# Performance work log

Measured on AMD Instinct MI355X. Metric: run time of the kernel, lower is better.

## Reference

```python
import jax, jax.numpy as jnp
import numpy as np

B, S, H = 16, 128, 768
L, K = 2, 4
NORM_ITEM = 0.5


def _xavier(key, shape):
    fan_in, fan_out = shape[-1], shape[-2]
    std = float(np.sqrt(2.0 / (fan_in + fan_out)))
    return jax.random.normal(key, shape, dtype=jnp.float32) * std


def setup_inputs() -> dict:
    key = jax.random.key(0)
    ks = jax.random.split(key, 13)
    sentences = jax.random.normal(ks[0], (B, S, H), dtype=jnp.float32)
    adj_matrix = jax.random.uniform(ks[1], (B, K, S, S), dtype=jnp.float32)
    return {
        "sentences": sentences,
        "adj_matrix": adj_matrix,
        # stacked per-(layer, dep_kind) parameters
        "W_in": _xavier(ks[2], (L, K, H, H)),
        "b_in": _xavier(ks[3], (L, K, H, 1)),
        "W_out": _xavier(ks[4], (L, K, H, H)),
        "b_out": _xavier(ks[5], (L, K, H, 1)),
        "Wg_in": _xavier(ks[6], (L, K, H, H)),
        "bg_in": _xavier(ks[7], (L, K, H, 1)),
        "Wg_out": _xavier(ks[8], (L, K, H, H)),
        "bg_out": _xavier(ks[9], (L, K, H, 1)),
        "W_loop": _xavier(ks[10], (L, H, H)),
    }


def reference(sentences, adj_matrix, W_in, b_in, W_out, b_out,
              Wg_in, bg_in, Wg_out, bg_out, W_loop):
    # sentences: [B,S,H], adj_matrix: [B,K,S,S]
    adj_in = adj_matrix                       # message along edges
    adj_out = jnp.swapaxes(adj_matrix, 2, 3)  # reversed edges
    h = jnp.swapaxes(sentences, 1, 2)         # [B,H,S]

    def conv(Wg, bg, W, b, adj, h):
        # Wg,W: [K,H,H]; bg,b: [K,H,1]; adj: [B,K,S,S]; h: [B,H,S]
        gate = jax.nn.sigmoid(jnp.einsum('khd,bds->bkhs', Wg, h) + bg[None])
        rel = NORM_ITEM * gate * (jnp.einsum('khd,bds->bkhs', W, h) + b[None])
        # bmm with adjacency, then sum over dep kinds
        return jnp.einsum('bkhs,bkst->bht', rel, adj)

    n_layers = W_in.shape[0]
    for l in range(n_layers):
        s = jnp.einsum('hd,bds->bhs', W_loop[l], h)  # self loop
        s = s + conv(Wg_in[l], bg_in[l], W_in[l], b_in[l], adj_in, h)
        s = s + conv(Wg_out[l], bg_out[l], W_out[l], b_out[l], adj_out, h)
        h = jax.nn.relu(s)
    return jnp.swapaxes(h, 1, 2)  # [B,S,H]
```

## Files before the change

### kernel.cpp

```cpp
#include <hip/hip_runtime.h>
#include <stdint.h>

#define B_ 16
#define S_ 128
#define H_ 768
#define K_ 4
#define L_ 2
#define T_ (B_*S_)

typedef __attribute__((ext_vector_type(4))) float f32x4;
typedef __attribute__((ext_vector_type(8))) short s16x8;
typedef __bf16 bf16x8 __attribute__((ext_vector_type(8)));
typedef unsigned short u16;

__device__ inline u16 f2bf(float f) {
    union { float f; uint32_t u; } v; v.f = f;
    uint32_t u = v.u;
    return (u16)((u + 0x7fffu + ((u >> 16) & 1u)) >> 16);
}

__device__ inline ushort4 f2bf4(float4 v) {
    ushort4 r; r.x = f2bf(v.x); r.y = f2bf(v.y); r.z = f2bf(v.z); r.w = f2bf(v.w);
    return r;
}

template <typename T>
__device__ inline auto mfma_impl(T a, T b, f32x4 c, int)
    -> decltype(__builtin_amdgcn_mfma_f32_16x16x32_bf16(a, b, c, 0, 0, 0)) {
    return __builtin_amdgcn_mfma_f32_16x16x32_bf16(a, b, c, 0, 0, 0);
}
template <typename T>
__device__ inline f32x4 mfma_impl(T a, T b, f32x4 c, long) {
    return __builtin_amdgcn_mfma_f32_16x16x32_bf16(
        __builtin_bit_cast(bf16x8, a), __builtin_bit_cast(bf16x8, b), c, 0, 0, 0);
}
__device__ inline f32x4 mfma16(s16x8 a, s16x8 b, f32x4 c) {
    return mfma_impl(a, b, c, 0);
}

__device__ inline void gload_lds16(const void* g, void* l) {
    __builtin_amdgcn_global_load_lds(
        (__attribute__((address_space(1))) void*)(g),
        (__attribute__((address_space(3))) void*)(l), 16, 0, 0);
}

__device__ inline void stage_tile(const char* gbase, int rowStrideBytes, u16* lds, int tid) {
    const int lane = tid & 63;
    const int w = tid >> 6;
    const int lr = lane >> 3;
    const int cb = (lane & 7) << 4;
    #pragma unroll
    for (int j = 0; j < 4; ++j) {
        const int seg = j * 4 + w;
        const int row = seg * 8 + lr;
        const int sb = cb ^ ((row & 7) << 4);
        gload_lds16(gbase + (size_t)row * rowStrideBytes + sb,
                    lds + seg * 512);
    }
}

__device__ inline void stage64(const char* gbase, int rowStrideBytes, char* lds, int tid) {
    const int lane = tid & 63;
    const int w = tid >> 6;
    const int lr = lane >> 3;
    const int cb = (lane & 7) << 4;
    #pragma unroll
    for (int j = 0; j < 2; ++j) {
        const int seg = j * 4 + w;
        const int row = seg * 8 + lr;
        const int sb = cb ^ ((row & 7) << 4);
        gload_lds16(gbase + (size_t)row * rowStrideBytes + sb,
                    lds + seg * 1024);
    }
}

__device__ inline void stage128(const char* gRow0, int rowStrideBytes, char* ldsBase, int tid) {
    const int lane = tid & 63;
    const int w = tid >> 6;
    const int lr = lane >> 3;
    #pragma unroll
    for (int j = 0; j < 2; ++j) {
        const int seg = w * 2 + j;
        const int row = seg * 8 + lr;
        const int sb = ((lane & 7) << 4) ^ ((row & 7) << 4);
        gload_lds16(gRow0 + (size_t)row * rowStrideBytes + sb,
                    ldsBase + seg * 1024);
    }
}

__device__ inline s16x8 read_frag(const u16* lds, int row, int colByte) {
    const int bir = colByte ^ ((row & 7) << 4);
    return *(const s16x8*)((const char*)lds + row * 128 + bir);
}

__global__ void prep_weights(const float* __restrict__ Wg_in, const float* __restrict__ Wg_out,
                             const float* __restrict__ W_in,  const float* __restrict__ W_out,
                             const float* __restrict__ W_loop, const float* __restrict__ sent,
                             u16* __restrict__ Wg_all, u16* __restrict__ W_all,
                             u16* __restrict__ Wl, u16* __restrict__ X0) {
    const int i4 = blockIdx.x * blockDim.x + threadIdx.x;
    const int NW4 = L_ * K_ * H_ * H_ / 4;
    const int KHH4 = K_ * H_ * H_ / 4;
    if (i4 < NW4) {
        const int l = i4 / KHH4;
        const int rem = i4 - l * KHH4;
        const int d0 = (l * 2) * KHH4 + rem;
        const int d1 = d0 + KHH4;
        ((ushort4*)Wg_all)[d0] = f2bf4(((const float4*)Wg_in)[i4]);
        ((ushort4*)Wg_all)[d1] = f2bf4(((const float4*)Wg_out)[i4]);
        ((ushort4*)W_all)[d0]  = f2bf4(((const float4*)W_in)[i4]);
        ((ushort4*)W_all)[d1]  = f2bf4(((const float4*)W_out)[i4]);
    }
    if (i4 < L_ * H_ * H_ / 4)  ((ushort4*)Wl)[i4] = f2bf4(((const float4*)W_loop)[i4]);
    if (i4 < T_ * H_ / 4)       ((ushort4*)X0)[i4] = f2bf4(((const float4*)sent)[i4]);
}

__global__ void prep_adj(const float* __restrict__ adj, u16* __restrict__ adjA) {
    const int idx = blockIdx.x * blockDim.x + threadIdx.x;
    const int s = idx & 127;
    const int t = (idx >> 7) & 127;
    const int b = (idx >> 14) & 15;
    const int p = idx >> 18;
    const int dir = p >> 2, k = p & 3;
    const float v = dir ? adj[(((size_t)b * K_ + k) * S_ + t) * S_ + s]
                        : adj[(((size_t)b * K_ + k) * S_ + s) * S_ + t];
    adjA[idx] = f2bf(v);
}

__global__ __launch_bounds__(512, 2)
void gemm1_kernel(const u16* __restrict__ Xb,
                  const u16* __restrict__ Wg_all, const u16* __restrict__ W_all,
                  const u16* __restrict__ Wl,
                  const float* __restrict__ bg_in, const float* __restrict__ bg_out,
                  const float* __restrict__ b_in,  const float* __restrict__ b_out,
                  int layer,
                  u16* __restrict__ Rel2, float* __restrict__ SBuf) {
    __shared__ __align__(16) char smem[131072];

    const int tid = threadIdx.x;
    const int lane = tid & 63;
    const int w = tid >> 6;
    const int wm = w >> 1;
    const int wn = w & 1;
    const int l15 = lane & 15;
    const int hi16 = (lane >> 4) << 4;
    const int p = blockIdx.z;
    const bool gated = (p < 8);
    if (!gated && blockIdx.x >= 3) return;
    const int m0 = blockIdx.y * 256;
    const int n0 = gated ? blockIdx.x * 128 : blockIdx.x * 256;

    const u16* Wr;
    const u16* Wg = nullptr;
    if (gated) {
        const int dir = p >> 2, k = p & 3;
        const size_t woff = ((size_t)(layer * 2 + dir) * K_ + k) * (size_t)(H_ * H_);
        Wg = Wg_all + woff;
        Wr = W_all + woff;
    } else {
        Wr = Wl + (size_t)layer * H_ * H_;
    }

    const char* gA  = (const char*)Xb + (size_t)m0 * (H_ * 2);
    const char* gBr = (const char*)Wr + (size_t)n0 * (H_ * 2);
    const char* gBg = gated ? ((const char*)Wg + (size_t)n0 * (H_ * 2))
                            : (gBr + (size_t)128 * (H_ * 2));

    auto STAGE = [&](int kt, int c) {
        char* base = smem + c * 65536;
        stage128(gA + (size_t)kt * 128, H_ * 2, base, tid);
        stage128(gA + (size_t)128 * (H_ * 2) + (size_t)kt * 128, H_ * 2, base + 16384, tid);
        stage128(gBr + (size_t)kt * 128, H_ * 2, base + 32768, tid);
        stage128(gBg + (size_t)kt * 128, H_ * 2, base + 49152, tid);
    };

    const f32x4 zf = {0.f, 0.f, 0.f, 0.f};
    f32x4 accr[4][4], accg[4][4];
    #pragma unroll
    for (int i = 0; i < 4; ++i)
        #pragma unroll
        for (int j = 0; j < 4; ++j) { accr[i][j] = zf; accg[i][j] = zf; }

    STAGE(0, 0);
    __syncthreads();

    for (int t = 0; t < 12; ++t) {
        const int c = t & 1;
        if (t < 11) STAGE(t + 1, c ^ 1);
        const u16* lA  = (const u16*)(smem + c * 65536);
        const u16* lBr = (const u16*)(smem + c * 65536 + 32768);
        const u16* lBg = (const u16*)(smem + c * 65536 + 49152);
        #pragma unroll
        for (int kq = 0; kq < 2; ++kq) {
            const int ck = kq * 64 + hi16;
            s16x8 a[4], br[4], bg[4];
            #pragma unroll
            for (int i = 0; i < 4; ++i)
                a[i] = read_frag(lA, wm * 64 + i * 16 + l15, ck);
            #pragma unroll
            for (int j = 0; j < 4; ++j)
                br[j] = read_frag(lBr, wn * 64 + j * 16 + l15, ck);
            #pragma unroll
            for (int j = 0; j < 4; ++j)
                bg[j] = read_frag(lBg, wn * 64 + j * 16 + l15, ck);
            #pragma unroll
            for (int i = 0; i < 4; ++i) {
                #pragma unroll
                for (int j = 0; j < 4; ++j) {
                    accr[i][j] = mfma16(a[i], br[j], accr[i][j]);
                    accg[i][j] = mfma16(a[i], bg[j], accg[i][j]);
                }
            }
        }
        __syncthreads();
    }

    if (gated) {
        const int dir = p >> 2, k = p & 3;
        const float* bgp = (dir ? bg_out : bg_in) + ((size_t)layer * K_ + k) * H_;
        const float* brp = (dir ? b_out  : b_in ) + ((size_t)layer * K_ + k) * H_;
        #pragma unroll
        for (int j = 0; j < 4; ++j) {
            const int h = n0 + wn * 64 + j * 16 + l15;
            const float bgv = bgp[h];
            const float brv = brp[h];
            #pragma unroll
            for (int i = 0; i < 4; ++i) {
                const int tl = wm * 64 + i * 16 + ((lane >> 4) << 2);
                const int b = blockIdx.y * 2 + (tl >> 7);
                const int s0 = tl & 127;
                u16 tmp[4];
                #pragma unroll
                for (int r = 0; r < 4; ++r) {
                    const float g = accg[i][j][r] + bgv;
                    const float v = accr[i][j][r] + brv;
                    tmp[r] = f2bf(0.5f * v / (1.f + __expf(-g)));
                }
                ushort4 pk; pk.x = tmp[0]; pk.y = tmp[1]; pk.z = tmp[2]; pk.w = tmp[3];
                *(ushort4*)(Rel2 + (((size_t)p * B_ + b) * H_ + h) * S_ + s0) = pk;
            }
        }
    } else {
        #pragma unroll
        for (int j = 0; j < 4; ++j) {
            const int h1 = n0 + wn * 64 + j * 16 + l15;
            const int h2 = h1 + 128;
            #pragma unroll
            for (int i = 0; i < 4; ++i) {
                const int tg = m0 + wm * 64 + i * 16 + ((lane >> 4) << 2);
                #pragma unroll
                for (int r = 0; r < 4; ++r) {
                    SBuf[(size_t)(tg + r) * H_ + h1] = accr[i][j][r];
                    SBuf[(size_t)(tg + r) * H_ + h2] = accg[i][j][r];
                }
            }
        }
    }
}

__global__ __launch_bounds__(256, 2)
void gemm2_kernel(const u16* __restrict__ adjA, const u16* __restrict__ Rel2,
                  const float* __restrict__ SBuf,
                  u16* __restrict__ Xn, float* __restrict__ Out, int lastLayer) {
    __shared__ __align__(16) char smem2[49152];

    const int tid = threadIdx.x;
    const int lane = tid & 63;
    const int w = tid >> 6;
    const int wm = w >> 1, wn = w & 1;
    const int l15 = lane & 15;
    const int hi16 = (lane >> 4) << 4;
    const int h0 = blockIdx.x * 64;
    const int b = blockIdx.y;

    auto STAGE = [&](int q, int c) {
        const int p = q >> 1, sc = q & 1;
        const char* Ab = (const char*)adjA + ((size_t)p * B_ + b) * (S_ * S_ * 2) + sc * 128;
        const char* Bb = (const char*)Rel2 + (((size_t)p * B_ + b) * H_ + h0) * (S_ * 2) + sc * 128;
        char* base = smem2 + c * 24576;
        stage_tile(Ab, S_ * 2, (u16*)base, tid);
        stage64(Bb, S_ * 2, base + 16384, tid);
    };

    const f32x4 zf = {0.f, 0.f, 0.f, 0.f};
    f32x4 acc[4][2];
    #pragma unroll
    for (int i = 0; i < 4; ++i)
        #pragma unroll
        for (int j = 0; j < 2; ++j) acc[i][j] = zf;

    STAGE(0, 0);
    __syncthreads();

    for (int q = 0; q < 16; ++q) {
        const int c = q & 1;
        if (q < 15) STAGE(q + 1, c ^ 1);
        const u16* lA = (const u16*)(smem2 + c * 24576);
        const u16* lB = (const u16*)(smem2 + c * 24576 + 16384);
        #pragma unroll
        for (int kq = 0; kq < 2; ++kq) {
            const int ck = kq * 64 + hi16;
            s16x8 a[4], bb[2];
            #pragma unroll
            for (int i = 0; i < 4; ++i)
                a[i] = read_frag(lA, wm * 64 + i * 16 + l15, ck);
            #pragma unroll
            for (int j = 0; j < 2; ++j)
                bb[j] = read_frag(lB, wn * 32 + j * 16 + l15, ck);
            #pragma unroll
            for (int i = 0; i < 4; ++i)
                #pragma unroll
                for (int j = 0; j < 2; ++j)
                    acc[i][j] = mfma16(a[i], bb[j], acc[i][j]);
        }
        __syncthreads();
    }

    #pragma unroll
    for (int i = 0; i < 4; ++i) {
        const int tl = wm * 64 + i * 16 + ((lane >> 4) << 2);
        #pragma unroll
        for (int j = 0; j < 2; ++j) {
            const int h = h0 + wn * 32 + j * 16 + l15;
            #pragma unroll
            for (int r = 0; r < 4; ++r) {
                const size_t t = (size_t)b * S_ + tl + r;
                float v = acc[i][j][r] + SBuf[t * H_ + h];
                v = fmaxf(v, 0.f);
                if (lastLayer) Out[t * H_ + h] = v;
                else           Xn[t * H_ + h] = f2bf(v);
            }
        }
    }
}

extern "C" void kernel_launch(void* const* d_in, const int* in_sizes, int n_in,
                              void* d_out, int out_size, void* d_ws, size_t ws_size,
                              hipStream_t stream) {
    const float* sent   = (const float*)d_in[0];
    const float* adj    = (const float*)d_in[1];
    const float* W_in   = (const float*)d_in[2];
    const float* b_in   = (const float*)d_in[3];
    const float* W_out  = (const float*)d_in[4];
    const float* b_out  = (const float*)d_in[5];
    const float* Wg_in  = (const float*)d_in[6];
    const float* bg_in  = (const float*)d_in[7];
    const float* Wg_out = (const float*)d_in[8];
    const float* bg_out = (const float*)d_in[9];
    const float* W_loop = (const float*)d_in[10];

    char* ws = (char*)d_ws;
    u16* Wg_all = (u16*)(ws);
    u16* W_all  = (u16*)(ws + 18874368);
    u16* Wl     = (u16*)(ws + 37748736);
    u16* adjA   = (u16*)(ws + 40108032);
    u16* X0     = (u16*)(ws + 44302336);
    u16* X1     = (u16*)(ws + 47448064);
    u16* Rel2   = (u16*)(ws + 50593792);
    float* SBuf = (float*)(ws + 75759616);

    prep_weights<<<4608, 256, 0, stream>>>(Wg_in, Wg_out, W_in, W_out, W_loop, sent,
                                           Wg_all, W_all, Wl, X0);
    prep_adj<<<8192, 256, 0, stream>>>(adj, adjA);

    u16* Xc = X0;
    u16* Xn = X1;
    for (int l = 0; l < L_; ++l) {
        gemm1_kernel<<<dim3(6, 8, 9), 512, 0, stream>>>(Xc, Wg_all, W_all, Wl,
                                                        bg_in, bg_out, b_in, b_out,
                                                        l, Rel2, SBuf);
        gemm2_kernel<<<dim3(12, 16), 256, 0, stream>>>(adjA, Rel2, SBuf, Xn,
                                                       (float*)d_out, l == L_ - 1);
        u16* t = Xc; Xc = Xn; Xn = t;
    }
}
```

Baseline: 165.2 us.

## Shrink gemm1 tiles to 128 rows with 32-wide K steps and 256 threads

Changes the first GEMM kernel from a 256x128 tile with 512 threads and a 64-element K step to a 128x128 tile with 256 threads and a 32-element K step. LDS use drops from 128KB to 48KB and the swizzled staging becomes unswizzled 64-byte rows. The grid is reordered so blockIdx.x indexes a batch and the grid doubles in block count. The aim is more resident blocks and better CU fill, at the cost of less A/B reuse per block, more barriers, and possible LDS bank conflicts from dropping the XOR swizzle.

```diff
diff --git a/kernel.cpp b/kernel.cpp
--- a/kernel.cpp
+++ b/kernel.cpp
@@ -74,23 +74,24 @@
     }
 }
 
-__device__ inline void stage128(const char* gRow0, int rowStrideBytes, char* ldsBase, int tid) {
-    const int lane = tid & 63;
-    const int w = tid >> 6;
-    const int lr = lane >> 3;
+__device__ inline void stage32x128(const char* g, int strideB, char* lds, int tid) {
+    const int lane = tid & 63;
+    const int w = tid >> 6;
     #pragma unroll
     for (int j = 0; j < 2; ++j) {
-        const int seg = w * 2 + j;
-        const int row = seg * 8 + lr;
-        const int sb = ((lane & 7) << 4) ^ ((row & 7) << 4);
-        gload_lds16(gRow0 + (size_t)row * rowStrideBytes + sb,
-                    ldsBase + seg * 1024);
+        const int r = j * 64 + w * 16 + (lane >> 2);
+        gload_lds16(g + (size_t)r * strideB + ((lane & 3) << 4),
+                    lds + j * 4096 + w * 1024);
     }
 }
 
 __device__ inline s16x8 read_frag(const u16* lds, int row, int colByte) {
     const int bir = colByte ^ ((row & 7) << 4);
     return *(const s16x8*)((const char*)lds + row * 128 + bir);
+}
+
+__device__ inline s16x8 rf32(const u16* lds, int row, int cb) {
+    return *(const s16x8*)((const char*)lds + row * 64 + cb);
 }
 
 __global__ void prep_weights(const float* __restrict__ Wg_in, const float* __restrict__ Wg_out,
@@ -127,7 +128,7 @@
     adjA[idx] = f2bf(v);
 }
 
-__global__ __launch_bounds__(512, 2)
+__global__ __launch_bounds__(256, 2)
 void gemm1_kernel(const u16* __restrict__ Xb,
                   const u16* __restrict__ Wg_all, const u16* __restrict__ W_all,
                   const u16* __restrict__ Wl,
@@ -135,7 +136,7 @@
                   const float* __restrict__ b_in,  const float* __restrict__ b_out,
                   int layer,
                   u16* __restrict__ Rel2, float* __restrict__ SBuf) {
-    __shared__ __align__(16) char smem[131072];
+    __shared__ __align__(16) char smem[49152];
 
     const int tid = threadIdx.x;
     const int lane = tid & 63;
@@ -146,9 +147,9 @@
     const int hi16 = (lane >> 4) << 4;
     const int p = blockIdx.z;
     const bool gated = (p < 8);
-    if (!gated && blockIdx.x >= 3) return;
-    const int m0 = blockIdx.y * 256;
-    const int n0 = gated ? blockIdx.x * 128 : blockIdx.x * 256;
+    if (!gated && blockIdx.y >= 3) return;
+    const int m0 = blockIdx.x * 128;
+    const int n0 = gated ? blockIdx.y * 128 : blockIdx.y * 256;
 
     const u16* Wr;
     const u16* Wg = nullptr;
@@ -167,11 +168,11 @@
                             : (gBr + (size_t)128 * (H_ * 2));
 
     auto STAGE = [&](int kt, int c) {
-        char* base = smem + c * 65536;
-        stage128(gA + (size_t)kt * 128, H_ * 2, base, tid);
-        stage128(gA + (size_t)128 * (H_ * 2) + (size_t)kt * 128, H_ * 2, base + 16384, tid);
-        stage128(gBr + (size_t)kt * 128, H_ * 2, base + 32768, tid);
-        stage128(gBg + (size_t)kt * 128, H_ * 2, base + 49152, tid);
+        char* base = smem + c * 24576;
+        const size_t kb = (size_t)kt * 64;
+        stage32x128(gA  + kb, H_ * 2, base,         tid);
+        stage32x128(gBr + kb, H_ * 2, base + 8192,  tid);
+        stage32x128(gBg + kb, H_ * 2, base + 16384, tid);
     };
 
     const f32x4 zf = {0.f, 0.f, 0.f, 0.f};
@@ -184,32 +185,28 @@
     STAGE(0, 0);
     __syncthreads();
 
-    for (int t = 0; t < 12; ++t) {
+    for (int t = 0; t < 24; ++t) {
         const int c = t & 1;
-        if (t < 11) STAGE(t + 1, c ^ 1);
-        const u16* lA  = (const u16*)(smem + c * 65536);
-        const u16* lBr = (const u16*)(smem + c * 65536 + 32768);
-        const u16* lBg = (const u16*)(smem + c * 65536 + 49152);
-        #pragma unroll
-        for (int kq = 0; kq < 2; ++kq) {
-            const int ck = kq * 64 + hi16;
-            s16x8 a[4], br[4], bg[4];
-            #pragma unroll
-            for (int i = 0; i < 4; ++i)
-                a[i] = read_frag(lA, wm * 64 + i * 16 + l15, ck);
-            #pragma unroll
-            for (int j = 0; j < 4; ++j)
-                br[j] = read_frag(lBr, wn * 64 + j * 16 + l15, ck);
-            #pragma unroll
-            for (int j = 0; j < 4; ++j)
-                bg[j] = read_frag(lBg, wn * 64 + j * 16 + l15, ck);
-            #pragma unroll
-            for (int i = 0; i < 4; ++i) {
-                #pragma unroll
-                for (int j = 0; j < 4; ++j) {
-                    accr[i][j] = mfma16(a[i], br[j], accr[i][j]);
-                    accg[i][j] = mfma16(a[i], bg[j], accg[i][j]);
-                }
+        if (t < 23) STAGE(t + 1, c ^ 1);
+        const u16* lA  = (const u16*)(smem + c * 24576);
+        const u16* lBr = (const u16*)(smem + c * 24576 + 8192);
+        const u16* lBg = (const u16*)(smem + c * 24576 + 16384);
+        s16x8 a[4], br[4], bg[4];
+        #pragma unroll
+        for (int i = 0; i < 4; ++i)
+            a[i] = rf32(lA, wm * 64 + i * 16 + l15, hi16);
+        #pragma unroll
+        for (int j = 0; j < 4; ++j)
+            br[j] = rf32(lBr, wn * 64 + j * 16 + l15, hi16);
+        #pragma unroll
+        for (int j = 0; j < 4; ++j)
+            bg[j] = rf32(lBg, wn * 64 + j * 16 + l15, hi16);
+        #pragma unroll
+        for (int i = 0; i < 4; ++i) {
+            #pragma unroll
+            for (int j = 0; j < 4; ++j) {
+                accr[i][j] = mfma16(a[i], br[j], accr[i][j]);
+                accg[i][j] = mfma16(a[i], bg[j], accg[i][j]);
             }
         }
         __syncthreads();
@@ -219,6 +216,7 @@
         const int dir = p >> 2, k = p & 3;
         const float* bgp = (dir ? bg_out : bg_in) + ((size_t)layer * K_ + k) * H_;
         const float* brp = (dir ? b_out  : b_in ) + ((size_t)layer * K_ + k) * H_;
+        const int b = blockIdx.x;
         #pragma unroll
         for (int j = 0; j < 4; ++j) {
             const int h = n0 + wn * 64 + j * 16 + l15;
@@ -226,9 +224,7 @@
             const float brv = brp[h];
             #pragma unroll
             for (int i = 0; i < 4; ++i) {
-                const int tl = wm * 64 + i * 16 + ((lane >> 4) << 2);
-                const int b = blockIdx.y * 2 + (tl >> 7);
-                const int s0 = tl & 127;
+                const int s0 = wm * 64 + i * 16 + ((lane >> 4) << 2);
                 u16 tmp[4];
                 #pragma unroll
                 for (int r = 0; r < 4; ++r) {
@@ -366,9 +362,9 @@
     u16* Xc = X0;
     u16* Xn = X1;
     for (int l = 0; l < L_; ++l) {
-        gemm1_kernel<<<dim3(6, 8, 9), 512, 0, stream>>>(Xc, Wg_all, W_all, Wl,
-                                                        bg_in, bg_out, b_in, b_out,
-                                                        l, Rel2, SBuf);
+        gemm1_kernel<<<dim3(16, 6, 9), 256, 0, stream>>>(Xc, Wg_all, W_all, Wl,
+                                                         bg_in, bg_out, b_in, b_out,
+                                                         l, Rel2, SBuf);
         gemm2_kernel<<<dim3(12, 16), 256, 0, stream>>>(adjA, Rel2, SBuf, Xn,
                                                        (float*)d_out, l == L_ - 1);
         u16* t = Xc; Xc = Xn; Xn = t;
```

New measurement: 179.1 us. +8.4%, slower.

## Fuse self-loop GEMM into adjacency GEMM and remap gemm1 block schedule

Applied to the files above, without the earlier changes.

The self-loop product W_loop·h moves out of gemm1 and into gemm2 as 12 extra K-steps that accumulate into the same registers before the adjacency steps. This removes the fp32 SBuf round trip (write in gemm1, read in gemm2) and the unbalanced extra blocks in gemm1. gemm1 becomes a 1-D grid of 384 blocks with a remapped task order and a 2x4 warp layout (8x2 fragments per warp). The cost is a longer serial K loop in gemm2, from 16 to 28 steps, on a grid of only 192 blocks.

```diff
diff --git a/kernel.cpp b/kernel.cpp
--- a/kernel.cpp
+++ b/kernel.cpp
@@ -25,53 +25,23 @@
 }
 
 template <typename T>
-__device__ inline auto mfma_impl(T a, T b, f32x4 c, int)
+__device__ inline auto mfma16_impl(T a, T b, f32x4 c, int)
     -> decltype(__builtin_amdgcn_mfma_f32_16x16x32_bf16(a, b, c, 0, 0, 0)) {
     return __builtin_amdgcn_mfma_f32_16x16x32_bf16(a, b, c, 0, 0, 0);
 }
 template <typename T>
-__device__ inline f32x4 mfma_impl(T a, T b, f32x4 c, long) {
+__device__ inline f32x4 mfma16_impl(T a, T b, f32x4 c, long) {
     return __builtin_amdgcn_mfma_f32_16x16x32_bf16(
         __builtin_bit_cast(bf16x8, a), __builtin_bit_cast(bf16x8, b), c, 0, 0, 0);
 }
 __device__ inline f32x4 mfma16(s16x8 a, s16x8 b, f32x4 c) {
-    return mfma_impl(a, b, c, 0);
+    return mfma16_impl(a, b, c, 0);
 }
 
 __device__ inline void gload_lds16(const void* g, void* l) {
     __builtin_amdgcn_global_load_lds(
         (__attribute__((address_space(1))) void*)(g),
         (__attribute__((address_space(3))) void*)(l), 16, 0, 0);
-}
-
-__device__ inline void stage_tile(const char* gbase, int rowStrideBytes, u16* lds, int tid) {
-    const int lane = tid & 63;
-    const int w = tid >> 6;
-    const int lr = lane >> 3;
-    const int cb = (lane & 7) << 4;
-    #pragma unroll
-    for (int j = 0; j < 4; ++j) {
-        const int seg = j * 4 + w;
-        const int row = seg * 8 + lr;
-        const int sb = cb ^ ((row & 7) << 4);
-        gload_lds16(gbase + (size_t)row * rowStrideBytes + sb,
-                    lds + seg * 512);
-    }
-}
-
-__device__ inline void stage64(const char* gbase, int rowStrideBytes, char* lds, int tid) {
-    const int lane = tid & 63;
-    const int w = tid >> 6;
-    const int lr = lane >> 3;
-    const int cb = (lane & 7) << 4;
-    #pragma unroll
-    for (int j = 0; j < 2; ++j) {
-        const int seg = j * 4 + w;
-        const int row = seg * 8 + lr;
-        const int sb = cb ^ ((row & 7) << 4);
-        gload_lds16(gbase + (size_t)row * rowStrideBytes + sb,
-                    lds + seg * 1024);
-    }
 }
 
 __device__ inline void stage128(const char* gRow0, int rowStrideBytes, char* ldsBase, int tid) {
@@ -85,6 +55,34 @@
         const int sb = ((lane & 7) << 4) ^ ((row & 7) << 4);
         gload_lds16(gRow0 + (size_t)row * rowStrideBytes + sb,
                     ldsBase + seg * 1024);
+    }
+}
+
+__device__ inline void stage_tile(const char* gbase, int rowStrideBytes, u16* lds, int tid) {
+    const int lane = tid & 63;
+    const int w = tid >> 6;
+    const int lr = lane >> 3;
+    const int cb = (lane & 7) << 4;
+    #pragma unroll
+    for (int j = 0; j < 4; ++j) {
+        const int seg = j * 4 + w;
+        const int row = seg * 8 + lr;
+        const int sb = cb ^ ((row & 7) << 4);
+        gload_lds16(gbase + (size_t)row * rowStrideBytes + sb, lds + seg * 512);
+    }
+}
+
+__device__ inline void stage64(const char* gbase, int rowStrideBytes, char* lds, int tid) {
+    const int lane = tid & 63;
+    const int w = tid >> 6;
+    const int lr = lane >> 3;
+    const int cb = (lane & 7) << 4;
+    #pragma unroll
+    for (int j = 0; j < 2; ++j) {
+        const int seg = j * 4 + w;
+        const int row = seg * 8 + lr;
+        const int sb = cb ^ ((row & 7) << 4);
+        gload_lds16(gbase + (size_t)row * rowStrideBytes + sb, lds + seg * 1024);
     }
 }
 
@@ -130,41 +128,33 @@
 __global__ __launch_bounds__(512, 2)
 void gemm1_kernel(const u16* __restrict__ Xb,
                   const u16* __restrict__ Wg_all, const u16* __restrict__ W_all,
-                  const u16* __restrict__ Wl,
                   const float* __restrict__ bg_in, const float* __restrict__ bg_out,
                   const float* __restrict__ b_in,  const float* __restrict__ b_out,
-                  int layer,
-                  u16* __restrict__ Rel2, float* __restrict__ SBuf) {
+                  int layer, u16* __restrict__ Rel2) {
     __shared__ __align__(16) char smem[131072];
 
     const int tid = threadIdx.x;
     const int lane = tid & 63;
     const int w = tid >> 6;
-    const int wm = w >> 1;
-    const int wn = w & 1;
+    const int wm = w >> 2;
+    const int wn = w & 3;
     const int l15 = lane & 15;
     const int hi16 = (lane >> 4) << 4;
-    const int p = blockIdx.z;
-    const bool gated = (p < 8);
-    if (!gated && blockIdx.x >= 3) return;
-    const int m0 = blockIdx.y * 256;
-    const int n0 = gated ? blockIdx.x * 128 : blockIdx.x * 256;
-
-    const u16* Wr;
-    const u16* Wg = nullptr;
-    if (gated) {
-        const int dir = p >> 2, k = p & 3;
-        const size_t woff = ((size_t)(layer * 2 + dir) * K_ + k) * (size_t)(H_ * H_);
-        Wg = Wg_all + woff;
-        Wr = W_all + woff;
-    } else {
-        Wr = Wl + (size_t)layer * H_ * H_;
-    }
-
+
+    const int bid = blockIdx.x;
+    const int task = (bid & 7) * 48 + (bid >> 3);
+    const int p = task / 48;
+    const int r = task % 48;
+    const int y = r >> 3;
+    const int m = r & 7;
+    const int m0 = m * 256;
+    const int n0 = y * 128;
+    const int dir = p >> 2, kk = p & 3;
+
+    const size_t woff = ((size_t)(layer * 2 + dir) * K_ + kk) * (size_t)(H_ * H_);
     const char* gA  = (const char*)Xb + (size_t)m0 * (H_ * 2);
-    const char* gBr = (const char*)Wr + (size_t)n0 * (H_ * 2);
-    const char* gBg = gated ? ((const char*)Wg + (size_t)n0 * (H_ * 2))
-                            : (gBr + (size_t)128 * (H_ * 2));
+    const char* gBr = (const char*)(W_all + woff)  + (size_t)n0 * (H_ * 2);
+    const char* gBg = (const char*)(Wg_all + woff) + (size_t)n0 * (H_ * 2);
 
     auto STAGE = [&](int kt, int c) {
         char* base = smem + c * 65536;
@@ -175,11 +165,11 @@
     };
 
     const f32x4 zf = {0.f, 0.f, 0.f, 0.f};
-    f32x4 accr[4][4], accg[4][4];
-    #pragma unroll
-    for (int i = 0; i < 4; ++i)
-        #pragma unroll
-        for (int j = 0; j < 4; ++j) { accr[i][j] = zf; accg[i][j] = zf; }
+    f32x4 accr[8][2], accg[8][2];
+    #pragma unroll
+    for (int i = 0; i < 8; ++i)
+        #pragma unroll
+        for (int j = 0; j < 2; ++j) { accr[i][j] = zf; accg[i][j] = zf; }
 
     STAGE(0, 0);
     __syncthreads();
@@ -193,20 +183,19 @@
         #pragma unroll
         for (int kq = 0; kq < 2; ++kq) {
             const int ck = kq * 64 + hi16;
-            s16x8 a[4], br[4], bg[4];
-            #pragma unroll
-            for (int i = 0; i < 4; ++i)
-                a[i] = read_frag(lA, wm * 64 + i * 16 + l15, ck);
-            #pragma unroll
-            for (int j = 0; j < 4; ++j)
-                br[j] = read_frag(lBr, wn * 64 + j * 16 + l15, ck);
-            #pragma unroll
-            for (int j = 0; j < 4; ++j)
-                bg[j] = read_frag(lBg, wn * 64 + j * 16 + l15, ck);
-            #pragma unroll
-            for (int i = 0; i < 4; ++i) {
+            s16x8 a[8], br[2], bg[2];
+            #pragma unroll
+            for (int i = 0; i < 8; ++i)
+                a[i] = read_frag(lA, wm * 128 + i * 16 + l15, ck);
+            #pragma unroll
+            for (int j = 0; j < 2; ++j) {
+                br[j] = read_frag(lBr, wn * 32 + j * 16 + l15, ck);
+                bg[j] = read_frag(lBg, wn * 32 + j * 16 + l15, ck);
+            }
+            #pragma unroll
+            for (int i = 0; i < 8; ++i) {
                 #pragma unroll
-                for (int j = 0; j < 4; ++j) {
+                for (int j = 0; j < 2; ++j) {
                     accr[i][j] = mfma16(a[i], br[j], accr[i][j]);
                     accg[i][j] = mfma16(a[i], bg[j], accg[i][j]);
                 }
@@ -215,52 +204,35 @@
         __syncthreads();
     }
 
-    if (gated) {
-        const int dir = p >> 2, k = p & 3;
-        const float* bgp = (dir ? bg_out : bg_in) + ((size_t)layer * K_ + k) * H_;
-        const float* brp = (dir ? b_out  : b_in ) + ((size_t)layer * K_ + k) * H_;
-        #pragma unroll
-        for (int j = 0; j < 4; ++j) {
-            const int h = n0 + wn * 64 + j * 16 + l15;
-            const float bgv = bgp[h];
-            const float brv = brp[h];
-            #pragma unroll
-            for (int i = 0; i < 4; ++i) {
-                const int tl = wm * 64 + i * 16 + ((lane >> 4) << 2);
-                const int b = blockIdx.y * 2 + (tl >> 7);
-                const int s0 = tl & 127;
-                u16 tmp[4];
-                #pragma unroll
-                for (int r = 0; r < 4; ++r) {
-                    const float g = accg[i][j][r] + bgv;
-                    const float v = accr[i][j][r] + brv;
-                    tmp[r] = f2bf(0.5f * v / (1.f + __expf(-g)));
-                }
-                ushort4 pk; pk.x = tmp[0]; pk.y = tmp[1]; pk.z = tmp[2]; pk.w = tmp[3];
-                *(ushort4*)(Rel2 + (((size_t)p * B_ + b) * H_ + h) * S_ + s0) = pk;
+    const float* bgp = (dir ? bg_out : bg_in) + ((size_t)layer * K_ + kk) * H_;
+    const float* brp = (dir ? b_out  : b_in ) + ((size_t)layer * K_ + kk) * H_;
+    #pragma unroll
+    for (int j = 0; j < 2; ++j) {
+        const int h = n0 + wn * 32 + j * 16 + l15;
+        const float bgv = bgp[h];
+        const float brv = brp[h];
+        #pragma unroll
+        for (int i = 0; i < 8; ++i) {
+            const int tl = wm * 128 + i * 16 + ((lane >> 4) << 2);
+            const int bidx = m * 2 + (tl >> 7);
+            const int s0 = tl & 127;
+            u16 tmp[4];
+            #pragma unroll
+            for (int rr = 0; rr < 4; ++rr) {
+                const float g = accg[i][j][rr] + bgv;
+                const float v = accr[i][j][rr] + brv;
+                tmp[rr] = f2bf(0.5f * v / (1.f + __expf(-g)));
             }
-        }
-    } else {
-        #pragma unroll
-        for (int j = 0; j < 4; ++j) {
-            const int h1 = n0 + wn * 64 + j * 16 + l15;
-            const int h2 = h1 + 128;
-            #pragma unroll
-            for (int i = 0; i < 4; ++i) {
-                const int tg = m0 + wm * 64 + i * 16 + ((lane >> 4) << 2);
-                #pragma unroll
-                for (int r = 0; r < 4; ++r) {
-                    SBuf[(size_t)(tg + r) * H_ + h1] = accr[i][j][r];
-                    SBuf[(size_t)(tg + r) * H_ + h2] = accg[i][j][r];
-                }
-            }
+            ushort4 pk; pk.x = tmp[0]; pk.y = tmp[1]; pk.z = tmp[2]; pk.w = tmp[3];
+            *(ushort4*)(Rel2 + (((size_t)p * B_ + bidx) * H_ + h) * S_ + s0) = pk;
         }
     }
 }
 
 __global__ __launch_bounds__(256, 2)
 void gemm2_kernel(const u16* __restrict__ adjA, const u16* __restrict__ Rel2,
-                  const float* __restrict__ SBuf,
+                  const u16* __restrict__ Xc, const u16* __restrict__ Wlb,
+                  int layer,
                   u16* __restrict__ Xn, float* __restrict__ Out, int lastLayer) {
     __shared__ __align__(16) char smem2[49152];
 
@@ -273,13 +245,22 @@
     const int h0 = blockIdx.x * 64;
     const int b = blockIdx.y;
 
+    const char* gX  = (const char*)Xc + ((size_t)b * S_) * (H_ * 2);
+    const char* gWl = (const char*)(Wlb + (size_t)layer * H_ * H_) + (size_t)h0 * (H_ * 2);
+
     auto STAGE = [&](int q, int c) {
-        const int p = q >> 1, sc = q & 1;
-        const char* Ab = (const char*)adjA + ((size_t)p * B_ + b) * (S_ * S_ * 2) + sc * 128;
-        const char* Bb = (const char*)Rel2 + (((size_t)p * B_ + b) * H_ + h0) * (S_ * 2) + sc * 128;
         char* base = smem2 + c * 24576;
-        stage_tile(Ab, S_ * 2, (u16*)base, tid);
-        stage64(Bb, S_ * 2, base + 16384, tid);
+        if (q < 12) {
+            stage_tile(gX + (size_t)q * 128, H_ * 2, (u16*)base, tid);
+            stage64(gWl + (size_t)q * 128, H_ * 2, base + 16384, tid);
+        } else {
+            const int qa = q - 12;
+            const int p = qa >> 1, sc = qa & 1;
+            const char* Ab = (const char*)adjA + ((size_t)p * B_ + b) * (S_ * S_ * 2) + sc * 128;
+            const char* Bb = (const char*)Rel2 + (((size_t)p * B_ + b) * H_ + h0) * (S_ * 2) + sc * 128;
+            stage_tile(Ab, S_ * 2, (u16*)base, tid);
+            stage64(Bb, S_ * 2, base + 16384, tid);
+        }
     };
 
     const f32x4 zf = {0.f, 0.f, 0.f, 0.f};
@@ -292,9 +273,9 @@
     STAGE(0, 0);
     __syncthreads();
 
-    for (int q = 0; q < 16; ++q) {
+    for (int q = 0; q < 28; ++q) {
         const int c = q & 1;
-        if (q < 15) STAGE(q + 1, c ^ 1);
+        if (q < 27) STAGE(q + 1, c ^ 1);
         const u16* lA = (const u16*)(smem2 + c * 24576);
         const u16* lB = (const u16*)(smem2 + c * 24576 + 16384);
         #pragma unroll
@@ -323,10 +304,9 @@
         for (int j = 0; j < 2; ++j) {
             const int h = h0 + wn * 32 + j * 16 + l15;
             #pragma unroll
-            for (int r = 0; r < 4; ++r) {
-                const size_t t = (size_t)b * S_ + tl + r;
-                float v = acc[i][j][r] + SBuf[t * H_ + h];
-                v = fmaxf(v, 0.f);
+            for (int rr = 0; rr < 4; ++rr) {
+                const size_t t = (size_t)b * S_ + tl + rr;
+                float v = fmaxf(acc[i][j][rr], 0.f);
                 if (lastLayer) Out[t * H_ + h] = v;
                 else           Xn[t * H_ + h] = f2bf(v);
             }
@@ -352,25 +332,24 @@
     char* ws = (char*)d_ws;
     u16* Wg_all = (u16*)(ws);
     u16* W_all  = (u16*)(ws + 18874368);
-    u16* Wl     = (u16*)(ws + 37748736);
+    u16* Wlb    = (u16*)(ws + 37748736);
     u16* adjA   = (u16*)(ws + 40108032);
     u16* X0     = (u16*)(ws + 44302336);
     u16* X1     = (u16*)(ws + 47448064);
     u16* Rel2   = (u16*)(ws + 50593792);
-    float* SBuf = (float*)(ws + 75759616);
 
     prep_weights<<<4608, 256, 0, stream>>>(Wg_in, Wg_out, W_in, W_out, W_loop, sent,
-                                           Wg_all, W_all, Wl, X0);
+                                           Wg_all, W_all, Wlb, X0);
     prep_adj<<<8192, 256, 0, stream>>>(adj, adjA);
 
     u16* Xc = X0;
     u16* Xn = X1;
     for (int l = 0; l < L_; ++l) {
-        gemm1_kernel<<<dim3(6, 8, 9), 512, 0, stream>>>(Xc, Wg_all, W_all, Wl,
-                                                        bg_in, bg_out, b_in, b_out,
-                                                        l, Rel2, SBuf);
-        gemm2_kernel<<<dim3(12, 16), 256, 0, stream>>>(adjA, Rel2, SBuf, Xn,
-                                                       (float*)d_out, l == L_ - 1);
+        gemm1_kernel<<<384, 512, 0, stream>>>(Xc, Wg_all, W_all,
+                                              bg_in, bg_out, b_in, b_out,
+                                              l, Rel2);
+        gemm2_kernel<<<dim3(12, 16), 256, 0, stream>>>(adjA, Rel2, Xc, Wlb, l,
+                                                       Xn, (float*)d_out, l == L_ - 1);
         u16* t = Xc; Xc = Xn; Xn = t;
     }
 }
```

After: 161.7 us. 1.02x faster.
